# Optimization experiments

Measured on AMD Instinct MI355X. Metric: run time of the kernel, lower is better.

## Reference

```python
import jax, jax.numpy as jnp
import numpy as np

B, LQ, LK, D, H, DK, DV = 4, 2048, 2048, 1024, 16, 64, 64
TEMP = float(np.sqrt(DK))
LN_EPS = 1e-5


def setup_inputs() -> dict:
    key = jax.random.key(0)
    ks = jax.random.split(key, 12)
    std_qk = float(np.sqrt(2.0 / (D + DK)))
    std_v = float(np.sqrt(2.0 / (D + DV)))
    std_fc = float(np.sqrt(2.0 / (H * DV + D)))  # xavier normal
    return {
        "q": jax.random.normal(ks[0], (B, LQ, D), jnp.float32),
        "k": jax.random.normal(ks[1], (B, LK, D), jnp.float32),
        "v": jax.random.normal(ks[2], (B, LK, D), jnp.float32),
        "key_padding_mask": jax.random.randint(ks[3], (B, LK), 0, 2) > 0,
        "Wq": jax.random.normal(ks[4], (D, H * DK), jnp.float32) * std_qk,
        "bq": jnp.zeros((H * DK,), jnp.float32),
        "Wk": jax.random.normal(ks[5], (D, H * DK), jnp.float32) * std_qk,
        "bk": jnp.zeros((H * DK,), jnp.float32),
        "Wv": jax.random.normal(ks[6], (D, H * DV), jnp.float32) * std_v,
        "bv": jnp.zeros((H * DV,), jnp.float32),
        "Wo": jax.random.normal(ks[7], (H * DV, D), jnp.float32) * std_fc,
        "bo": jnp.zeros((D,), jnp.float32),
        "ln_g": jnp.ones((D,), jnp.float32),
        "ln_b": jnp.zeros((D,), jnp.float32),
    }


def reference(q, k, v, key_padding_mask, Wq, bq, Wk, bk, Wv, bv, Wo, bo, ln_g, ln_b):
    residual = q
    # projections -> [B, H, L, dh]
    qh = (q @ Wq + bq).reshape(B, LQ, H, DK).transpose(0, 2, 1, 3)
    kh = (k @ Wk + bk).reshape(B, LK, H, DK).transpose(0, 2, 1, 3)
    vh = (v @ Wv + bv).reshape(B, LK, H, DV).transpose(0, 2, 1, 3)
    # scaled dot-product attention, mask padded keys with -inf pre-softmax
    logits = jnp.einsum("bhqd,bhkd->bhqk", qh, kh) / TEMP
    logits = jnp.where(key_padding_mask[:, None, None, :], -jnp.inf, logits)
    attn = jax.nn.softmax(logits, axis=-1)  # masked entries -> 0
    out = jnp.einsum("bhqk,bhkd->bhqd", attn, vh)
    # concat heads (head-major per original permute) -> [B, LQ, H*DV]
    out = out.transpose(0, 2, 1, 3).reshape(B, LQ, H * DV)
    out = out @ Wo + bo
    out = out + residual  # skip connection (d_out == d_model)
    # LayerNorm over last dim
    mu = out.mean(-1, keepdims=True)
    var = ((out - mu) ** 2).mean(-1, keepdims=True)
    out = (out - mu) * jax.lax.rsqrt(var + LN_EPS) * ln_g + ln_b
    attn_avg = attn.mean(axis=1)  # average over heads -> [B, LQ, LK]
    return out, attn_avg
```

## Files before the change

### kernel.cpp

```cpp
#include <hip/hip_runtime.h>
#include <hip/hip_bf16.h>
#include <math.h>

#define B_    4
#define LQ_   2048
#define LK_   2048
#define D_    1024
#define H_    16
#define LN_EPS_ 1e-5f
#define NEGINF (-__builtin_inff())
#define QSCALE 0.18033688011112042f

typedef __attribute__((ext_vector_type(8))) short bf16x8;
typedef __attribute__((ext_vector_type(4))) short bf16x4;
typedef __attribute__((ext_vector_type(4))) float f32x4;

#define MFMA(a, b, c) __builtin_amdgcn_mfma_f32_16x16x32_bf16(a, b, c, 0, 0, 0)

#if __has_builtin(__builtin_amdgcn_exp2f)
#define EXP2(x) __builtin_amdgcn_exp2f(x)
#else
#define EXP2(x) __expf((x) * 0.6931471805599453f)
#endif

__device__ __forceinline__ short f2bf(float f) {
    union { __hip_bfloat16 h; short s; } u;
    u.h = __float2bfloat16(f);
    return u.s;
}

__device__ __forceinline__ void gld16(const short* g, short* l) {
    __builtin_amdgcn_global_load_lds(
        (const __attribute__((address_space(1))) void*)g,
        (__attribute__((address_space(3))) void*)l, 16, 0, 0);
}

__global__ __launch_bounds__(256) void scan_kernel(
    const int* __restrict__ mask, int* __restrict__ idx, int* __restrict__ pos,
    int* __restrict__ cnt, float* __restrict__ maskc)
{
    const int b = blockIdx.x;
    const int t = threadIdx.x;
    const int lane = t & 63, wid = t >> 6;
    __shared__ int wsum[4];
    const int base = b * 2048 + t * 8;

    int fl[8]; int loc = 0;
    #pragma unroll
    for (int j = 0; j < 8; ++j) { fl[j] = (mask[base + j] == 0) ? 1 : 0; loc += fl[j]; }

    int inc = loc;
    #pragma unroll
    for (int d = 1; d < 64; d <<= 1) {
        const int n = __shfl_up(inc, d);
        if (lane >= d) inc += n;
    }
    if (lane == 63) wsum[wid] = inc;
    __syncthreads();
    int wbase = 0;
    for (int i = 0; i < wid; ++i) wbase += wsum[i];
    const int total = wsum[0] + wsum[1] + wsum[2] + wsum[3];

    int e = wbase + inc - loc;
    #pragma unroll
    for (int j = 0; j < 8; ++j) {
        const int p = t * 8 + j;
        if (fl[j]) { idx[b * 2048 + e] = p; pos[base + j] = e; ++e; }
        else        pos[base + j] = -1;
        maskc[base + j] = (p < total) ? 0.f : NEGINF;
        if (p >= total) idx[base + j] = 0;
    }
    if (t == 0) cnt[b] = total;
}

__global__ __launch_bounds__(256) void cast_x_kernel(
    const float* __restrict__ q, const float* __restrict__ k, const float* __restrict__ v,
    const int* __restrict__ mask,
    short* __restrict__ Xq, short* __restrict__ Xk, short* __restrict__ Xv,
    float* __restrict__ maskf)
{
    const int which = blockIdx.y;
    const float* src = which == 0 ? q : (which == 1 ? k : v);
    short* dst       = which == 0 ? Xq : (which == 1 ? Xk : Xv);
    const int t = threadIdx.x;
    const size_t i = ((size_t)blockIdx.x * 256 + t) * 8;
    const float4 a = *reinterpret_cast<const float4*>(src + i);
    const float4 c = *reinterpret_cast<const float4*>(src + i + 4);
    bf16x8 o;
    o[0] = f2bf(a.x); o[1] = f2bf(a.y); o[2] = f2bf(a.z); o[3] = f2bf(a.w);
    o[4] = f2bf(c.x); o[5] = f2bf(c.y); o[6] = f2bf(c.z); o[7] = f2bf(c.w);
    *reinterpret_cast<bf16x8*>(dst + i) = o;
    if (which == 0) {
        const int gid = blockIdx.x * 256 + t;
        if (gid < B_ * LK_) maskf[gid] = (mask[gid] != 0) ? NEGINF : 0.0f;
    }
}

__global__ __launch_bounds__(256) void cast_wt_kernel(
    const float* __restrict__ Wq, const float* __restrict__ Wk,
    const float* __restrict__ Wv, const float* __restrict__ Wo,
    short* __restrict__ Wtq, short* __restrict__ Wtk,
    short* __restrict__ Wtv, short* __restrict__ Wto)
{
    const int which = blockIdx.z;
    const float* W = which == 0 ? Wq : (which == 1 ? Wk : (which == 2 ? Wv : Wo));
    short* Wt      = which == 0 ? Wtq : (which == 1 ? Wtk : (which == 2 ? Wtv : Wto));

    __shared__ float T[64][65];
    const int t = threadIdx.x;
    const int k0 = blockIdx.x * 64, n0 = blockIdx.y * 64;
    {
        const int row = t >> 2, cq = (t & 3) * 16;
        #pragma unroll
        for (int i = 0; i < 4; ++i) {
            const float4 v4 = *reinterpret_cast<const float4*>(&W[(size_t)(k0 + row) * 1024 + n0 + cq + i * 4]);
            T[row][cq + i * 4 + 0] = v4.x; T[row][cq + i * 4 + 1] = v4.y;
            T[row][cq + i * 4 + 2] = v4.z; T[row][cq + i * 4 + 3] = v4.w;
        }
    }
    __syncthreads();
    const int nl = t >> 2, kq = (t & 3) * 16;
    bf16x8 o0, o1;
    #pragma unroll
    for (int j = 0; j < 8; ++j) {
        o0[j] = f2bf(T[kq + j][nl]);
        o1[j] = f2bf(T[kq + 8 + j][nl]);
    }
    *reinterpret_cast<bf16x8*>(&Wt[(size_t)(n0 + nl) * 1024 + k0 + kq]) = o0;
    *reinterpret_cast<bf16x8*>(&Wt[(size_t)(n0 + nl) * 1024 + k0 + kq + 8]) = o1;
}

__global__ __launch_bounds__(256) void proj_kernel(
    const short* __restrict__ Xq, const short* __restrict__ Xk, const short* __restrict__ Xv,
    const short* __restrict__ Wtq, const short* __restrict__ Wtk, const short* __restrict__ Wtv,
    const float* __restrict__ bq, const float* __restrict__ bk, const float* __restrict__ bv,
    const int* __restrict__ pos,
    short* __restrict__ qh, short* __restrict__ kh, short* __restrict__ vTc)
{
    const int which = blockIdx.z;
    const short* A  = which == 0 ? Xq : (which == 1 ? Xk : Xv);
    const short* Bt = which == 0 ? Wtq : (which == 1 ? Wtk : Wtv);
    const float* bias = which == 0 ? bq : (which == 1 ? bk : bv);

    __shared__ short Al[4096];
    __shared__ short Bl[4096];

    const int t = threadIdx.x;
    const int lane = t & 63, w = t >> 6;
    const int wm = w >> 1, wn = w & 1;
    const int g = lane >> 4, r16 = lane & 15;
    const int m0 = blockIdx.y * 128, n0 = blockIdx.x * 128;

    f32x4 acc[4][4] = {};

    for (int k0 = 0; k0 < 1024; k0 += 32) {
        __syncthreads();
        #pragma unroll
        for (int i = 0; i < 2; ++i) {
            const int row = i * 64 + (t >> 2);
            const int cl = (t & 3) ^ ((row >> 1) & 3);
            gld16(A  + (size_t)(m0 + row) * 1024 + k0 + cl * 8, Al + i * 2048 + t * 8);
            gld16(Bt + (size_t)(n0 + row) * 1024 + k0 + cl * 8, Bl + i * 2048 + t * 8);
        }
        __syncthreads();

        bf16x8 af[4], bf[4];
        #pragma unroll
        for (int mf = 0; mf < 4; ++mf) {
            const int row = wm * 64 + mf * 16 + r16;
            af[mf] = *reinterpret_cast<const bf16x8*>(
                (const char*)Al + row * 64 + (((g ^ ((row >> 1) & 3))) << 4));
        }
        #pragma unroll
        for (int nf = 0; nf < 4; ++nf) {
            const int row = wn * 64 + nf * 16 + r16;
            bf[nf] = *reinterpret_cast<const bf16x8*>(
                (const char*)Bl + row * 64 + (((g ^ ((row >> 1) & 3))) << 4));
        }
        #pragma unroll
        for (int mf = 0; mf < 4; ++mf)
            #pragma unroll
            for (int nf = 0; nf < 4; ++nf)
                acc[mf][nf] = MFMA(af[mf], bf[nf], acc[mf][nf]);
    }

    if (which < 2) {
        #pragma unroll
        for (int nf = 0; nf < 4; ++nf) {
            const int n = n0 + wn * 64 + nf * 16 + r16;
            const int h = n >> 6, dh = n & 63;
            const float bn = bias[n];
            #pragma unroll
            for (int mf = 0; mf < 4; ++mf) {
                #pragma unroll
                for (int r = 0; r < 4; ++r) {
                    const int m = m0 + wm * 64 + mf * 16 + 4 * g + r;
                    const int bb = m >> 11, l = m & 2047;
                    float vf = acc[mf][nf][r] + bn;
                    if (which == 0) vf *= QSCALE;
                    ((which == 0) ? qh : kh)[(((size_t)(bb * H_ + h)) * LQ_ + l) * 64 + dh] = f2bf(vf);
                }
            }
        }
    } else {
        int posr[4][4], bbr[4][4];
        #pragma unroll
        for (int mf = 0; mf < 4; ++mf)
            #pragma unroll
            for (int r = 0; r < 4; ++r) {
                const int m = m0 + wm * 64 + mf * 16 + 4 * g + r;
                const int bb = m >> 11, l = m & 2047;
                bbr[mf][r] = bb;
                posr[mf][r] = pos[bb * 2048 + l];
            }
        #pragma unroll
        for (int nf = 0; nf < 4; ++nf) {
            const int n = n0 + wn * 64 + nf * 16 + r16;
            const int h = n >> 6, dh = n & 63;
            const float bn = bias[n];
            #pragma unroll
            for (int mf = 0; mf < 4; ++mf) {
                #pragma unroll
                for (int r = 0; r < 4; ++r) {
                    const int pc = posr[mf][r];
                    if (pc >= 0)
                        vTc[(((size_t)(bbr[mf][r] * H_ + h)) * 64 + dh) * (size_t)LK_ + pc] =
                            f2bf(acc[mf][nf][r] + bn);
                }
            }
        }
    }
}

__global__ __launch_bounds__(256) void flash_kernel(
    const short* __restrict__ qh, const short* __restrict__ kh, const short* __restrict__ vTc,
    const int* __restrict__ idx, const int* __restrict__ cnt, const float* __restrict__ maskc,
    short* __restrict__ ctx, float* __restrict__ mOut, float* __restrict__ sOut)
{
    const int q0 = blockIdx.x * 64;
    const int h  = blockIdx.y;
    const int b  = blockIdx.z;

    __shared__ short Kl[2][4096];
    __shared__ short Vl[2][4096];

    const int t = threadIdx.x;
    const int lane = t & 63, w = t >> 6;
    const int g = lane >> 4, q16 = lane & 15;

    const short* kbase = kh + (size_t)(b * H_ + h) * LK_ * 64;
    const short* vbase = vTc + (size_t)(b * H_ + h) * 64 * (size_t)LK_;
    const int*   idxb  = idx + b * 2048;
    const int nt = (cnt[b] + 63) >> 6;

    bf16x8 qf0, qf1;
    {
        const short* qrow = qh + ((size_t)(b * H_ + h) * LQ_ + q0 + w * 16 + q16) * 64;
        qf0 = *reinterpret_cast<const bf16x8*>(qrow + 8 * g);
        qf1 = *reinterpret_cast<const bf16x8*>(qrow + 32 + 8 * g);
    }

    f32x4 mlast[4] = {};
    if (nt > 0) {
        #pragma unroll
        for (int kb = 0; kb < 4; ++kb)
            mlast[kb] = *reinterpret_cast<const f32x4*>(
                maskc + b * 2048 + (nt - 1) * 64 + kb * 16 + 4 * g);
    }

    const int srw = t >> 3, scl = t & 7;

    f32x4 ot[4] = {};
    float m_run = NEGINF, l_run = 0.f;

    if (nt > 0) {
        #pragma unroll
        for (int i = 0; i < 2; ++i) {
            const int row = i * 32 + srw;
            const int cl = scl ^ (row & 7);
            const int orig = idxb[row];
            gld16(kbase + (size_t)orig * 64 + cl * 8, Kl[0] + i * 2048 + t * 8);
            gld16(vbase + (size_t)row * LK_ + cl * 8, Vl[0] + i * 2048 + t * 8);
        }
    }
    __syncthreads();

    int cur = 0;
    for (int kt = 0; kt < nt; ++kt) {
        if (kt + 1 < nt) {
            const int kn = (kt + 1) * 64;
            #pragma unroll
            for (int i = 0; i < 2; ++i) {
                const int row = i * 32 + srw;
                const int cl = scl ^ (row & 7);
                const int orig = idxb[kn + row];
                gld16(kbase + (size_t)orig * 64 + cl * 8, Kl[cur ^ 1] + i * 2048 + t * 8);
                gld16(vbase + (size_t)row * LK_ + kn + cl * 8, Vl[cur ^ 1] + i * 2048 + t * 8);
            }
        }
        const bool lastt = (kt == nt - 1);

        float lg[4][4];
        const short* klp = Kl[cur];
        __builtin_amdgcn_s_setprio(1);
        #pragma unroll
        for (int kb = 0; kb < 4; ++kb) {
            const int krow = kb * 16 + q16;
            const char* rowp = (const char*)klp + krow * 128;
            const int sw = (krow & 7) << 4;
            const bf16x8 kf0 = *reinterpret_cast<const bf16x8*>(rowp + ((g << 4) ^ sw));
            const bf16x8 kf1 = *reinterpret_cast<const bf16x8*>(rowp + (((4 + g) << 4) ^ sw));
            f32x4 s = lastt ? mlast[kb] : (f32x4){0.f, 0.f, 0.f, 0.f};
            s = MFMA(kf0, qf0, s);
            s = MFMA(kf1, qf1, s);
            #pragma unroll
            for (int r = 0; r < 4; ++r) lg[kb][r] = s[r];
        }
        __builtin_amdgcn_s_setprio(0);

        float tm = NEGINF;
        #pragma unroll
        for (int kb = 0; kb < 4; ++kb)
            #pragma unroll
            for (int r = 0; r < 4; ++r) tm = fmaxf(tm, lg[kb][r]);
        tm = fmaxf(tm, __shfl_xor(tm, 16));
        tm = fmaxf(tm, __shfl_xor(tm, 32));

        const bool skip = __all(tm <= m_run + 8.0f);
        if (!skip) {
            const float m_new = fmaxf(m_run, tm);
            const float alpha = (m_run == NEGINF) ? 0.f : EXP2(m_run - m_new);
            #pragma unroll
            for (int fc = 0; fc < 4; ++fc)
                #pragma unroll
                for (int r = 0; r < 4; ++r) ot[fc][r] *= alpha;
            l_run *= alpha;
            m_run = m_new;
        }
        const float m_use = (m_run == NEGINF) ? 0.f : m_run;

        float p[4][4];
        float ls = 0.f;
        #pragma unroll
        for (int kb = 0; kb < 4; ++kb)
            #pragma unroll
            for (int r = 0; r < 4; ++r) { p[kb][r] = EXP2(lg[kb][r] - m_use); ls += p[kb][r]; }
        ls += __shfl_xor(ls, 16);
        ls += __shfl_xor(ls, 32);
        l_run += ls;

        bf16x8 pb[2];
        #pragma unroll
        for (int r = 0; r < 4; ++r) {
            pb[0][r]     = f2bf(p[0][r]);
            pb[0][4 + r] = f2bf(p[1][r]);
            pb[1][r]     = f2bf(p[2][r]);
            pb[1][4 + r] = f2bf(p[3][r]);
        }

        const short* vlp = Vl[cur];
        __builtin_amdgcn_s_setprio(1);
        #pragma unroll
        for (int fc = 0; fc < 4; ++fc) {
            const int dvrow = fc * 16 + q16;
            const char* rowp = (const char*)vlp + dvrow * 128;
            const int sw = (dvrow & 7) << 4;
            #pragma unroll
            for (int tt = 0; tt < 2; ++tt) {
                const bf16x4 va = *reinterpret_cast<const bf16x4*>(rowp + ((64 * tt + 8 * g) ^ sw));
                const bf16x4 vb = *reinterpret_cast<const bf16x4*>(rowp + ((64 * tt + 32 + 8 * g) ^ sw));
                bf16x8 af;
                af[0] = va[0]; af[1] = va[1]; af[2] = va[2]; af[3] = va[3];
                af[4] = vb[0]; af[5] = vb[1]; af[6] = vb[2]; af[7] = vb[3];
                ot[fc] = MFMA(af, pb[tt], ot[fc]);
            }
        }
        __builtin_amdgcn_s_setprio(0);

        __syncthreads();
        cur ^= 1;
    }

    const float rs = (l_run > 0.f) ? 1.0f / l_run : 0.f;
    short* crow = ctx + ((size_t)b * LQ_ + q0 + w * 16 + q16) * (size_t)(H_ * 64) + h * 64;
    #pragma unroll
    for (int fc = 0; fc < 4; ++fc) {
        bf16x4 o4;
        #pragma unroll
        for (int r = 0; r < 4; ++r) o4[r] = f2bf(ot[fc][r] * rs);
        *reinterpret_cast<bf16x4*>(crow + fc * 16 + 4 * g) = o4;
    }
    if (lane < 16) {
        const size_t idxo = (size_t)(b * H_ + h) * LQ_ + q0 + w * 16 + lane;
        mOut[idxo] = m_run;
        sOut[idxo] = l_run;
    }
}

__global__ __launch_bounds__(256) void avg_kernel(
    const short* __restrict__ qh, const short* __restrict__ kh,
    const float* __restrict__ maskf,
    const float* __restrict__ mS, const float* __restrict__ sS,
    float* __restrict__ attn_avg)
{
    const int k0 = blockIdx.x * 64;
    const int q0 = blockIdx.y * 64;
    const int b  = blockIdx.z;

    __shared__ short Kl[2][4096];

    const int t = threadIdx.x;
    const int lane = t & 63, w = t >> 6;
    const int g = lane >> 4, q16 = lane & 15;

    f32x4 mk[4];
    #pragma unroll
    for (int kb = 0; kb < 4; ++kb)
        mk[kb] = *reinterpret_cast<const f32x4*>(maskf + b * LK_ + k0 + kb * 16 + 4 * g);

    const int srw = t >> 3, scl = t & 7;
    const size_t khbase = (size_t)b * H_ * (size_t)LK_ * 64;

    const short* qbase = qh + ((size_t)b * H_ * LQ_ + q0 + w * 16 + q16) * 64;
    const size_t stbase = (size_t)b * H_ * LQ_ + q0 + w * 16 + q16;

    {
        #pragma unroll
        for (int i = 0; i < 2; ++i) {
            const int row = i * 32 + srw;
            const int cl = scl ^ (row & 7);
            gld16(kh + khbase + (size_t)(k0 + row) * 64 + cl * 8, Kl[0] + i * 2048 + t * 8);
        }
    }
    bf16x8 qf0 = *reinterpret_cast<const bf16x8*>(qbase + 8 * g);
    bf16x8 qf1 = *reinterpret_cast<const bf16x8*>(qbase + 32 + 8 * g);
    float mrow = mS[stbase], srv = sS[stbase];
    __syncthreads();

    f32x4 acc[4] = {};
    int cur = 0;
    for (int hh = 0; hh < H_; ++hh) {
        bf16x8 qn0, qn1; float mn = 0.f, sn = 0.f;
        if (hh + 1 < H_) {
            #pragma unroll
            for (int i = 0; i < 2; ++i) {
                const int row = i * 32 + srw;
                const int cl = scl ^ (row & 7);
                gld16(kh + khbase + (size_t)(hh + 1) * LK_ * 64 + (size_t)(k0 + row) * 64 + cl * 8,
                      Kl[cur ^ 1] + i * 2048 + t * 8);
            }
            const short* qb2 = qbase + (size_t)(hh + 1) * LQ_ * 64;
            qn0 = *reinterpret_cast<const bf16x8*>(qb2 + 8 * g);
            qn1 = *reinterpret_cast<const bf16x8*>(qb2 + 32 + 8 * g);
            mn = mS[stbase + (size_t)(hh + 1) * LQ_];
            sn = sS[stbase + (size_t)(hh + 1) * LQ_];
        }

        const float valid = (mrow == NEGINF || srv <= 0.f) ? 0.f : 1.0f / srv;
        const float m_use = (mrow == NEGINF) ? 0.f : mrow;

        const short* klp = Kl[cur];
        __builtin_amdgcn_s_setprio(1);
        #pragma unroll
        for (int kb = 0; kb < 4; ++kb) {
            const int krow = kb * 16 + q16;
            const char* rowp = (const char*)klp + krow * 128;
            const int sw = (krow & 7) << 4;
            const bf16x8 kf0 = *reinterpret_cast<const bf16x8*>(rowp + ((g << 4) ^ sw));
            const bf16x8 kf1 = *reinterpret_cast<const bf16x8*>(rowp + (((4 + g) << 4) ^ sw));
            f32x4 s = mk[kb];
            s = MFMA(kf0, qf0, s);
            s = MFMA(kf1, qf1, s);
            #pragma unroll
            for (int r = 0; r < 4; ++r)
                acc[kb][r] += EXP2(s[r] - m_use) * valid;
        }
        __builtin_amdgcn_s_setprio(0);

        __syncthreads();
        if (hh + 1 < H_) { qf0 = qn0; qf1 = qn1; mrow = mn; srv = sn; }
        cur ^= 1;
    }

    const float sc = 1.0f / (float)H_;
    float* orow = attn_avg + ((size_t)b * LQ_ + q0 + w * 16 + q16) * (size_t)LK_ + k0;
    #pragma unroll
    for (int kb = 0; kb < 4; ++kb) {
        f32x4 o = acc[kb];
        o[0] *= sc; o[1] *= sc; o[2] *= sc; o[3] *= sc;
        *reinterpret_cast<f32x4*>(orow + kb * 16 + 4 * g) = o;
    }
}

__global__ __launch_bounds__(256) void outproj_kernel(
    const short* __restrict__ ctxIn, const short* __restrict__ Wto,
    const float* __restrict__ bo, const float* __restrict__ resid,
    float* __restrict__ preln)
{
    __shared__ short Al[4096];
    __shared__ short Bl[4096];

    const int t = threadIdx.x;
    const int lane = t & 63, w = t >> 6;
    const int wm = w >> 1, wn = w & 1;
    const int g = lane >> 4, r16 = lane & 15;
    const int m0 = blockIdx.y * 128, n0 = blockIdx.x * 128;

    f32x4 acc[4][4] = {};

    for (int k0 = 0; k0 < 1024; k0 += 32) {
        __syncthreads();
        #pragma unroll
        for (int i = 0; i < 2; ++i) {
            const int row = i * 64 + (t >> 2);
            const int cl = (t & 3) ^ ((row >> 1) & 3);
            gld16(ctxIn + (size_t)(m0 + row) * 1024 + k0 + cl * 8, Al + i * 2048 + t * 8);
            gld16(Wto   + (size_t)(n0 + row) * 1024 + k0 + cl * 8, Bl + i * 2048 + t * 8);
        }
        __syncthreads();

        bf16x8 af[4], bf[4];
        #pragma unroll
        for (int mf = 0; mf < 4; ++mf) {
            const int row = wm * 64 + mf * 16 + r16;
            af[mf] = *reinterpret_cast<const bf16x8*>(
                (const char*)Al + row * 64 + (((g ^ ((row >> 1) & 3))) << 4));
        }
        #pragma unroll
        for (int nf = 0; nf < 4; ++nf) {
            const int row = wn * 64 + nf * 16 + r16;
            bf[nf] = *reinterpret_cast<const bf16x8*>(
                (const char*)Bl + row * 64 + (((g ^ ((row >> 1) & 3))) << 4));
        }
        #pragma unroll
        for (int mf = 0; mf < 4; ++mf)
            #pragma unroll
            for (int nf = 0; nf < 4; ++nf)
                acc[mf][nf] = MFMA(af[mf], bf[nf], acc[mf][nf]);
    }

    #pragma unroll
    for (int nf = 0; nf < 4; ++nf) {
        const int n = n0 + wn * 64 + nf * 16 + r16;
        const float bn = bo[n];
        #pragma unroll
        for (int mf = 0; mf < 4; ++mf) {
            #pragma unroll
            for (int r = 0; r < 4; ++r) {
                const size_t m = m0 + wm * 64 + mf * 16 + 4 * g + r;
                preln[m * 1024 + n] = acc[mf][nf][r] + bn + resid[m * 1024 + n];
            }
        }
    }
}

__global__ __launch_bounds__(256) void ln_kernel(
    const float* __restrict__ xin, const float* __restrict__ gam,
    const float* __restrict__ bet, float* __restrict__ out)
{
    const size_t row = blockIdx.x;
    const int t = threadIdx.x;
    const float4 v = *reinterpret_cast<const float4*>(&xin[row * 1024 + t * 4]);

    float s  = v.x + v.y + v.z + v.w;
    float ss = v.x * v.x + v.y * v.y + v.z * v.z + v.w * v.w;
    #pragma unroll
    for (int w = 1; w < 64; w <<= 1) { s += __shfl_xor(s, w); ss += __shfl_xor(ss, w); }

    __shared__ float rs_[4], rss_[4];
    if ((t & 63) == 0) { rs_[t >> 6] = s; rss_[t >> 6] = ss; }
    __syncthreads();
    s  = rs_[0] + rs_[1] + rs_[2] + rs_[3];
    ss = rss_[0] + rss_[1] + rss_[2] + rss_[3];

    const float mean = s * (1.0f / 1024.0f);
    const float var  = ss * (1.0f / 1024.0f) - mean * mean;
    const float rstd = rsqrtf(var + LN_EPS_);

    const float4 g4 = *reinterpret_cast<const float4*>(&gam[t * 4]);
    const float4 b4 = *reinterpret_cast<const float4*>(&bet[t * 4]);
    float4 o;
    o.x = (v.x - mean) * rstd * g4.x + b4.x;
    o.y = (v.y - mean) * rstd * g4.y + b4.y;
    o.z = (v.z - mean) * rstd * g4.z + b4.z;
    o.w = (v.w - mean) * rstd * g4.w + b4.w;
    *reinterpret_cast<float4*>(&out[row * 1024 + t * 4]) = o;
}

extern "C" void kernel_launch(void* const* d_in, const int* in_sizes, int n_in,
                              void* d_out, int out_size, void* d_ws, size_t ws_size,
                              hipStream_t stream)
{
    const float* q    = (const float*)d_in[0];
    const float* k    = (const float*)d_in[1];
    const float* v    = (const float*)d_in[2];
    const int*   mask = (const int*)d_in[3];
    const float* Wq   = (const float*)d_in[4];
    const float* bq   = (const float*)d_in[5];
    const float* Wk   = (const float*)d_in[6];
    const float* bk   = (const float*)d_in[7];
    const float* Wv   = (const float*)d_in[8];
    const float* bv   = (const float*)d_in[9];
    const float* Wo   = (const float*)d_in[10];
    const float* bo   = (const float*)d_in[11];
    const float* lng  = (const float*)d_in[12];
    const float* lnb  = (const float*)d_in[13];

    float* out      = (float*)d_out;
    float* attn_avg = out + (size_t)B_ * LQ_ * D_;

    const size_t XSZ = (size_t)B_ * LQ_ * D_;
    const size_t WSZ = (size_t)D_ * D_;

    short* Xq  = (short*)d_ws;
    short* Xk  = Xq + XSZ;
    short* Xv  = Xk + XSZ;
    short* Wtq = Xv + XSZ;
    short* Wtk = Wtq + WSZ;
    short* Wtv = Wtk + WSZ;
    short* Wto = Wtv + WSZ;
    short* qh  = Wto + WSZ;
    short* kh  = qh + XSZ;
    short* vTc = kh + XSZ;
    float* mSt = (float*)(vTc + XSZ);
    float* sSt = mSt + (size_t)B_ * H_ * LQ_;
    float* maskf = sSt + (size_t)B_ * H_ * LQ_;
    float* maskc = maskf + (size_t)B_ * LK_;
    int*   idx   = (int*)(maskc + (size_t)B_ * LK_);
    int*   pos   = idx + (size_t)B_ * LK_;
    int*   cnt   = pos + (size_t)B_ * LK_;
    float* preln = (float*)qh;
    short* ctx   = Xv;

    scan_kernel<<<dim3(B_), 256, 0, stream>>>(mask, idx, pos, cnt, maskc);
    cast_x_kernel<<<dim3(4096, 3), 256, 0, stream>>>(q, k, v, mask, Xq, Xk, Xv, maskf);
    cast_wt_kernel<<<dim3(16, 16, 4), 256, 0, stream>>>(Wq, Wk, Wv, Wo, Wtq, Wtk, Wtv, Wto);

    proj_kernel<<<dim3(8, 64, 3), 256, 0, stream>>>(Xq, Xk, Xv, Wtq, Wtk, Wtv,
                                                    bq, bk, bv, pos, qh, kh, vTc);

    flash_kernel<<<dim3(32, 16, 4), 256, 0, stream>>>(qh, kh, vTc, idx, cnt, maskc,
                                                      ctx, mSt, sSt);

    avg_kernel<<<dim3(32, 32, 4), 256, 0, stream>>>(qh, kh, maskf, mSt, sSt, attn_avg);

    outproj_kernel<<<dim3(8, 64), 256, 0, stream>>>(ctx, Wto, bo, q, preln);

    ln_kernel<<<8192, 256, 0, stream>>>(preln, lng, lnb, out);
}
```

Before: 325.5 us.

## Compact unmasked keys in head-average kernel and zero-fill masked columns

The head-averaged attention kernel now walks only the compacted list of unmasked keys, using the index list from the scan kernel. Blocks past the valid count exit early, and results are scattered back to their original columns. Masked columns are zeroed up front by a new full-size fill kernel. The per-element normalisation multiply is folded into the exponent offset. This removes roughly half of the MFMA/exp work for a random mask, at the cost of an extra full write of the output and scattered, uncoalesced stores.

New measurement: 367.9 us. 1.13x slower.

```diff
diff --git a/kernel.cpp b/kernel.cpp
--- a/kernel.cpp
+++ b/kernel.cpp
@@ -35,6 +35,12 @@
         (__attribute__((address_space(3))) void*)l, 16, 0, 0);
 }
 
+__global__ __launch_bounds__(256) void zfill_kernel(float* __restrict__ p)
+{
+    const size_t i = ((size_t)blockIdx.x * 256 + threadIdx.x) * 4;
+    *reinterpret_cast<f32x4*>(p + i) = (f32x4){0.f, 0.f, 0.f, 0.f};
+}
+
 __global__ __launch_bounds__(256) void scan_kernel(
     const int* __restrict__ mask, int* __restrict__ idx, int* __restrict__ pos,
     int* __restrict__ cnt, float* __restrict__ maskc)
@@ -75,9 +81,7 @@
 
 __global__ __launch_bounds__(256) void cast_x_kernel(
     const float* __restrict__ q, const float* __restrict__ k, const float* __restrict__ v,
-    const int* __restrict__ mask,
-    short* __restrict__ Xq, short* __restrict__ Xk, short* __restrict__ Xv,
-    float* __restrict__ maskf)
+    short* __restrict__ Xq, short* __restrict__ Xk, short* __restrict__ Xv)
 {
     const int which = blockIdx.y;
     const float* src = which == 0 ? q : (which == 1 ? k : v);
@@ -90,10 +94,6 @@
     o[0] = f2bf(a.x); o[1] = f2bf(a.y); o[2] = f2bf(a.z); o[3] = f2bf(a.w);
     o[4] = f2bf(c.x); o[5] = f2bf(c.y); o[6] = f2bf(c.z); o[7] = f2bf(c.w);
     *reinterpret_cast<bf16x8*>(dst + i) = o;
-    if (which == 0) {
-        const int gid = blockIdx.x * 256 + t;
-        if (gid < B_ * LK_) maskf[gid] = (mask[gid] != 0) ? NEGINF : 0.0f;
-    }
 }
 
 __global__ __launch_bounds__(256) void cast_wt_kernel(
@@ -399,13 +399,18 @@
 
 __global__ __launch_bounds__(256) void avg_kernel(
     const short* __restrict__ qh, const short* __restrict__ kh,
-    const float* __restrict__ maskf,
+    const int* __restrict__ idx, const int* __restrict__ cnt,
+    const float* __restrict__ maskc,
     const float* __restrict__ mS, const float* __restrict__ sS,
     float* __restrict__ attn_avg)
 {
-    const int k0 = blockIdx.x * 64;
-    const int q0 = blockIdx.y * 64;
-    const int b  = blockIdx.z;
+    const int b = blockIdx.z;
+    const int cntb = cnt[b];
+    const int nt = (cntb + 63) >> 6;
+    if ((int)blockIdx.x >= nt) return;
+
+    const int kc0 = blockIdx.x * 64;
+    const int q0  = blockIdx.y * 64;
 
     __shared__ short Kl[2][4096];
 
@@ -416,21 +421,22 @@
     f32x4 mk[4];
     #pragma unroll
     for (int kb = 0; kb < 4; ++kb)
-        mk[kb] = *reinterpret_cast<const f32x4*>(maskf + b * LK_ + k0 + kb * 16 + 4 * g);
+        mk[kb] = *reinterpret_cast<const f32x4*>(maskc + b * 2048 + kc0 + kb * 16 + 4 * g);
 
     const int srw = t >> 3, scl = t & 7;
     const size_t khbase = (size_t)b * H_ * (size_t)LK_ * 64;
+    const int* idxb = idx + b * 2048;
+
+    const int orig0 = idxb[kc0 + srw];
+    const int orig1 = idxb[kc0 + 32 + srw];
+    const int cl = scl ^ (srw & 7);
 
     const short* qbase = qh + ((size_t)b * H_ * LQ_ + q0 + w * 16 + q16) * 64;
     const size_t stbase = (size_t)b * H_ * LQ_ + q0 + w * 16 + q16;
 
     {
-        #pragma unroll
-        for (int i = 0; i < 2; ++i) {
-            const int row = i * 32 + srw;
-            const int cl = scl ^ (row & 7);
-            gld16(kh + khbase + (size_t)(k0 + row) * 64 + cl * 8, Kl[0] + i * 2048 + t * 8);
-        }
+        gld16(kh + khbase + (size_t)orig0 * 64 + cl * 8, Kl[0] + t * 8);
+        gld16(kh + khbase + (size_t)orig1 * 64 + cl * 8, Kl[0] + 2048 + t * 8);
     }
     bf16x8 qf0 = *reinterpret_cast<const bf16x8*>(qbase + 8 * g);
     bf16x8 qf1 = *reinterpret_cast<const bf16x8*>(qbase + 32 + 8 * g);
@@ -442,13 +448,9 @@
     for (int hh = 0; hh < H_; ++hh) {
         bf16x8 qn0, qn1; float mn = 0.f, sn = 0.f;
         if (hh + 1 < H_) {
-            #pragma unroll
-            for (int i = 0; i < 2; ++i) {
-                const int row = i * 32 + srw;
-                const int cl = scl ^ (row & 7);
-                gld16(kh + khbase + (size_t)(hh + 1) * LK_ * 64 + (size_t)(k0 + row) * 64 + cl * 8,
-                      Kl[cur ^ 1] + i * 2048 + t * 8);
-            }
+            const size_t hb = khbase + (size_t)(hh + 1) * LK_ * 64;
+            gld16(kh + hb + (size_t)orig0 * 64 + cl * 8, Kl[cur ^ 1] + t * 8);
+            gld16(kh + hb + (size_t)orig1 * 64 + cl * 8, Kl[cur ^ 1] + 2048 + t * 8);
             const short* qb2 = qbase + (size_t)(hh + 1) * LQ_ * 64;
             qn0 = *reinterpret_cast<const bf16x8*>(qb2 + 8 * g);
             qn1 = *reinterpret_cast<const bf16x8*>(qb2 + 32 + 8 * g);
@@ -456,8 +458,8 @@
             sn = sS[stbase + (size_t)(hh + 1) * LQ_];
         }
 
-        const float valid = (mrow == NEGINF || srv <= 0.f) ? 0.f : 1.0f / srv;
-        const float m_use = (mrow == NEGINF) ? 0.f : mrow;
+        const float madj = (mrow == NEGINF || srv <= 0.f)
+                               ? __builtin_inff() : mrow + __log2f(srv);
 
         const short* klp = Kl[cur];
         __builtin_amdgcn_s_setprio(1);
@@ -473,7 +475,7 @@
             s = MFMA(kf1, qf1, s);
             #pragma unroll
             for (int r = 0; r < 4; ++r)
-                acc[kb][r] += EXP2(s[r] - m_use) * valid;
+                acc[kb][r] += EXP2(s[r] - madj);
         }
         __builtin_amdgcn_s_setprio(0);
 
@@ -483,12 +485,14 @@
     }
 
     const float sc = 1.0f / (float)H_;
-    float* orow = attn_avg + ((size_t)b * LQ_ + q0 + w * 16 + q16) * (size_t)LK_ + k0;
+    float* orow = attn_avg + ((size_t)b * LQ_ + q0 + w * 16 + q16) * (size_t)LK_;
     #pragma unroll
     for (int kb = 0; kb < 4; ++kb) {
-        f32x4 o = acc[kb];
-        o[0] *= sc; o[1] *= sc; o[2] *= sc; o[3] *= sc;
-        *reinterpret_cast<f32x4*>(orow + kb * 16 + 4 * g) = o;
+        #pragma unroll
+        for (int r = 0; r < 4; ++r) {
+            const int kc = kc0 + kb * 16 + 4 * g + r;
+            if (kc < cntb) orow[idxb[kc]] = acc[kb][r] * sc;
+        }
     }
 }
 
@@ -624,16 +628,16 @@
     short* vTc = kh + XSZ;
     float* mSt = (float*)(vTc + XSZ);
     float* sSt = mSt + (size_t)B_ * H_ * LQ_;
-    float* maskf = sSt + (size_t)B_ * H_ * LQ_;
-    float* maskc = maskf + (size_t)B_ * LK_;
+    float* maskc = sSt + (size_t)B_ * H_ * LQ_;
     int*   idx   = (int*)(maskc + (size_t)B_ * LK_);
     int*   pos   = idx + (size_t)B_ * LK_;
     int*   cnt   = pos + (size_t)B_ * LK_;
     float* preln = (float*)qh;
     short* ctx   = Xv;
 
+    zfill_kernel<<<dim3((B_ * LQ_ * LK_) / (256 * 4)), 256, 0, stream>>>(attn_avg);
     scan_kernel<<<dim3(B_), 256, 0, stream>>>(mask, idx, pos, cnt, maskc);
-    cast_x_kernel<<<dim3(4096, 3), 256, 0, stream>>>(q, k, v, mask, Xq, Xk, Xv, maskf);
+    cast_x_kernel<<<dim3(4096, 3), 256, 0, stream>>>(q, k, v, Xq, Xk, Xv);
     cast_wt_kernel<<<dim3(16, 16, 4), 256, 0, stream>>>(Wq, Wk, Wv, Wo, Wtq, Wtk, Wtv, Wto);
 
     proj_kernel<<<dim3(8, 64, 3), 256, 0, stream>>>(Xq, Xk, Xv, Wtq, Wtk, Wtv,
@@ -642,7 +646,8 @@
     flash_kernel<<<dim3(32, 16, 4), 256, 0, stream>>>(qh, kh, vTc, idx, cnt, maskc,
                                                       ctx, mSt, sSt);
 
-    avg_kernel<<<dim3(32, 32, 4), 256, 0, stream>>>(qh, kh, maskf, mSt, sSt, attn_avg);
+    avg_kernel<<<dim3(32, 32, 4), 256, 0, stream>>>(qh, kh, idx, cnt, maskc,
+                                                    mSt, sSt, attn_avg);
 
     outproj_kernel<<<dim3(8, 64), 256, 0, stream>>>(ctx, Wto, bo, q, preln);
 
```

## Process four heads per pipeline stage in attention-average kernel and fold normalizer into exponent

Applied to the files above, without the earlier changes.

The head-averaging kernel now stages K tiles, Q fragments and softmax stats for four heads at a time in a double-buffered LDS array, so it runs 4 barrier-separated stages instead of 16. This cuts synchronisation count and gives more independent MFMA/exp work between barriers. The 1/sum multiply is folded into the exponent by subtracting log2(sum) from the max, which removes a multiply per element. In exchange LDS use grows fourfold (64 KB) and register pressure rises, which may lower occupancy.

Result: slower. 376.5 us (+15.7%).

```diff
diff --git a/kernel.cpp b/kernel.cpp
--- a/kernel.cpp
+++ b/kernel.cpp
@@ -407,7 +407,7 @@
     const int q0 = blockIdx.y * 64;
     const int b  = blockIdx.z;
 
-    __shared__ short Kl[2][4096];
+    __shared__ short Kl[2][4][4096];
 
     const int t = threadIdx.x;
     const int lane = t & 63, w = t >> 6;
@@ -419,75 +419,84 @@
         mk[kb] = *reinterpret_cast<const f32x4*>(maskf + b * LK_ + k0 + kb * 16 + 4 * g);
 
     const int srw = t >> 3, scl = t & 7;
-    const size_t khbase = (size_t)b * H_ * (size_t)LK_ * 64;
-
+    const int cl = scl ^ (srw & 7);
+    const short* kbb = kh + ((size_t)b * H_ * LK_ + k0) * 64;
     const short* qbase = qh + ((size_t)b * H_ * LQ_ + q0 + w * 16 + q16) * 64;
     const size_t stbase = (size_t)b * H_ * LQ_ + q0 + w * 16 + q16;
 
-    {
-        #pragma unroll
-        for (int i = 0; i < 2; ++i) {
-            const int row = i * 32 + srw;
-            const int cl = scl ^ (row & 7);
-            gld16(kh + khbase + (size_t)(k0 + row) * 64 + cl * 8, Kl[0] + i * 2048 + t * 8);
-        }
-    }
-    bf16x8 qf0 = *reinterpret_cast<const bf16x8*>(qbase + 8 * g);
-    bf16x8 qf1 = *reinterpret_cast<const bf16x8*>(qbase + 32 + 8 * g);
-    float mrow = mS[stbase], srv = sS[stbase];
+    bf16x8 qc[4][2], qn[4][2];
+    float mc[4], sc[4], mn[4], sn[4];
+
+    #pragma unroll
+    for (int hi = 0; hi < 4; ++hi) {
+        const short* kp = kbb + (size_t)hi * LK_ * 64;
+        gld16(kp + (size_t)srw * 64 + cl * 8,        &Kl[0][hi][0] + t * 8);
+        gld16(kp + (size_t)(32 + srw) * 64 + cl * 8, &Kl[0][hi][2048] + t * 8);
+        const short* qp = qbase + (size_t)hi * LQ_ * 64;
+        qc[hi][0] = *reinterpret_cast<const bf16x8*>(qp + 8 * g);
+        qc[hi][1] = *reinterpret_cast<const bf16x8*>(qp + 32 + 8 * g);
+        mc[hi] = mS[stbase + (size_t)hi * LQ_];
+        sc[hi] = sS[stbase + (size_t)hi * LQ_];
+    }
     __syncthreads();
 
     f32x4 acc[4] = {};
-    int cur = 0;
-    for (int hh = 0; hh < H_; ++hh) {
-        bf16x8 qn0, qn1; float mn = 0.f, sn = 0.f;
-        if (hh + 1 < H_) {
-            #pragma unroll
-            for (int i = 0; i < 2; ++i) {
-                const int row = i * 32 + srw;
-                const int cl = scl ^ (row & 7);
-                gld16(kh + khbase + (size_t)(hh + 1) * LK_ * 64 + (size_t)(k0 + row) * 64 + cl * 8,
-                      Kl[cur ^ 1] + i * 2048 + t * 8);
-            }
-            const short* qb2 = qbase + (size_t)(hh + 1) * LQ_ * 64;
-            qn0 = *reinterpret_cast<const bf16x8*>(qb2 + 8 * g);
-            qn1 = *reinterpret_cast<const bf16x8*>(qb2 + 32 + 8 * g);
-            mn = mS[stbase + (size_t)(hh + 1) * LQ_];
-            sn = sS[stbase + (size_t)(hh + 1) * LQ_];
-        }
-
-        const float valid = (mrow == NEGINF || srv <= 0.f) ? 0.f : 1.0f / srv;
-        const float m_use = (mrow == NEGINF) ? 0.f : mrow;
-
-        const short* klp = Kl[cur];
+
+    for (int e = 0; e < 4; ++e) {
+        if (e < 3) {
+            const short* kbuf = (e & 1) ? &Kl[0][0][0] : &Kl[1][0][0];
+            #pragma unroll
+            for (int hi = 0; hi < 4; ++hi) {
+                const int h = (e + 1) * 4 + hi;
+                const short* kp = kbb + (size_t)h * LK_ * 64;
+                gld16(kp + (size_t)srw * 64 + cl * 8,        (short*)kbuf + hi * 4096 + t * 8);
+                gld16(kp + (size_t)(32 + srw) * 64 + cl * 8, (short*)kbuf + hi * 4096 + 2048 + t * 8);
+                const short* qp = qbase + (size_t)h * LQ_ * 64;
+                qn[hi][0] = *reinterpret_cast<const bf16x8*>(qp + 8 * g);
+                qn[hi][1] = *reinterpret_cast<const bf16x8*>(qp + 32 + 8 * g);
+                mn[hi] = mS[stbase + (size_t)h * LQ_];
+                sn[hi] = sS[stbase + (size_t)h * LQ_];
+            }
+        }
+
+        const short* cbuf = (e & 1) ? &Kl[1][0][0] : &Kl[0][0][0];
         __builtin_amdgcn_s_setprio(1);
         #pragma unroll
-        for (int kb = 0; kb < 4; ++kb) {
-            const int krow = kb * 16 + q16;
-            const char* rowp = (const char*)klp + krow * 128;
-            const int sw = (krow & 7) << 4;
-            const bf16x8 kf0 = *reinterpret_cast<const bf16x8*>(rowp + ((g << 4) ^ sw));
-            const bf16x8 kf1 = *reinterpret_cast<const bf16x8*>(rowp + (((4 + g) << 4) ^ sw));
-            f32x4 s = mk[kb];
-            s = MFMA(kf0, qf0, s);
-            s = MFMA(kf1, qf1, s);
-            #pragma unroll
-            for (int r = 0; r < 4; ++r)
-                acc[kb][r] += EXP2(s[r] - m_use) * valid;
+        for (int hi = 0; hi < 4; ++hi) {
+            const float madj = (mc[hi] == NEGINF || sc[hi] <= 0.f)
+                                   ? __builtin_inff() : mc[hi] + __log2f(sc[hi]);
+            const short* klp = cbuf + hi * 4096;
+            #pragma unroll
+            for (int kb = 0; kb < 4; ++kb) {
+                const int krow = kb * 16 + q16;
+                const char* rowp = (const char*)klp + krow * 128;
+                const int sw = (krow & 7) << 4;
+                const bf16x8 kf0 = *reinterpret_cast<const bf16x8*>(rowp + ((g << 4) ^ sw));
+                const bf16x8 kf1 = *reinterpret_cast<const bf16x8*>(rowp + (((4 + g) << 4) ^ sw));
+                f32x4 s = mk[kb];
+                s = MFMA(kf0, qc[hi][0], s);
+                s = MFMA(kf1, qc[hi][1], s);
+                #pragma unroll
+                for (int r = 0; r < 4; ++r)
+                    acc[kb][r] += EXP2(s[r] - madj);
+            }
         }
         __builtin_amdgcn_s_setprio(0);
 
         __syncthreads();
-        if (hh + 1 < H_) { qf0 = qn0; qf1 = qn1; mrow = mn; srv = sn; }
-        cur ^= 1;
-    }
-
-    const float sc = 1.0f / (float)H_;
+        #pragma unroll
+        for (int hi = 0; hi < 4; ++hi) {
+            qc[hi][0] = qn[hi][0]; qc[hi][1] = qn[hi][1];
+            mc[hi] = mn[hi]; sc[hi] = sn[hi];
+        }
+    }
+
+    const float scale = 1.0f / (float)H_;
     float* orow = attn_avg + ((size_t)b * LQ_ + q0 + w * 16 + q16) * (size_t)LK_ + k0;
     #pragma unroll
     for (int kb = 0; kb < 4; ++kb) {
         f32x4 o = acc[kb];
-        o[0] *= sc; o[1] *= sc; o[2] *= sc; o[3] *= sc;
+        o[0] *= scale; o[1] *= scale; o[2] *= scale; o[3] *= scale;
         *reinterpret_cast<f32x4*>(orow + kb * 16 + 4 * g) = o;
     }
 }
```
